# Kernel optimization log

Hardware: AMD Instinct MI355X
Metric: run time of the kernel (lower is better)

Reference implementation:

```python
import jax, jax.numpy as jnp
import numpy as np

N_NODES = 50000
N_EDGES = 800000
IN_DIM = 128
HID = 256
N_CLASSES = 10
N_GRAPHS = 64
BN_EPS = 1e-5


def setup_inputs() -> dict:
    key = jax.random.key(0)
    ks = jax.random.split(key, 12)
    x = jax.random.normal(ks[0], (N_NODES, IN_DIM), dtype=jnp.float32)
    edge_index = jax.random.randint(ks[1], (2, N_EDGES), 0, N_NODES, dtype=jnp.int32)
    batch = jnp.sort(jax.random.randint(ks[2], (N_NODES,), 0, N_GRAPHS, dtype=jnp.int32))
    def glorot(k, fi, fo):
        s = jnp.sqrt(6.0 / (fi + fo))
        return jax.random.uniform(k, (fi, fo), jnp.float32, -s, s)
    return {
        "x": x, "edge_index": edge_index, "batch": batch,
        "W1": glorot(ks[3], IN_DIM, HID), "b1": jnp.zeros((HID,), jnp.float32),
        "W2": glorot(ks[4], HID, HID),    "b2": jnp.zeros((HID,), jnp.float32),
        "W3": glorot(ks[5], HID, HID),    "b3": jnp.zeros((HID,), jnp.float32),
        "g1": jnp.ones((HID,), jnp.float32), "be1": jnp.zeros((HID,), jnp.float32),
        "g2": jnp.ones((HID,), jnp.float32), "be2": jnp.zeros((HID,), jnp.float32),
        "Wf": glorot(ks[6], HID, N_CLASSES), "bf": jnp.zeros((N_CLASSES,), jnp.float32),
    }


def _gcn_conv(h_in, W, b, src, dst, dis):
    # GCNConv: D^{-1/2}(A+I)D^{-1/2} (X W) + b, dis = deg^{-1/2} with self-loops
    h = h_in @ W                                    # [N, C]
    norm = (dis[src] * dis[dst])[:, None]           # [E, 1]
    agg = jax.ops.segment_sum(h[src] * norm, dst, num_segments=N_NODES)
    agg = agg + h * (dis * dis)[:, None]            # self-loop contribution
    return agg + b


def _batch_norm(h, gamma, beta):
    mu = jnp.mean(h, axis=0)
    var = jnp.mean(jnp.square(h - mu), axis=0)      # biased, as torch training BN
    return (h - mu) * jax.lax.rsqrt(var + BN_EPS) * gamma + beta


def reference(x, edge_index, batch, W1, b1, W2, b2, W3, b3, g1, be1, g2, be2, Wf, bf):
    src, dst = edge_index[0], edge_index[1]
    # symmetric degree with self-loops (unit edge weights)
    deg = 1.0 + jax.ops.segment_sum(jnp.ones((N_EDGES,), jnp.float32), dst, num_segments=N_NODES)
    dis = jax.lax.rsqrt(deg)
    h = jax.nn.relu(_gcn_conv(x, W1, b1, src, dst, dis))
    h = jax.nn.relu(_gcn_conv(h, W2, b2, src, dst, dis))
    h = _batch_norm(h, g1, be1)
    h = jax.nn.relu(_gcn_conv(h, W3, b3, src, dst, dis))
    h = _batch_norm(h, g2, be2)
    # global mean pool over graphs
    sums = jax.ops.segment_sum(h, batch, num_segments=N_GRAPHS)
    cnts = jax.ops.segment_sum(jnp.ones((N_NODES,), jnp.float32), batch, num_segments=N_GRAPHS)
    pooled = sums / jnp.maximum(cnts, 1.0)[:, None]  # [G, HID]
    return pooled @ Wf + bf
```

## Files before the change

### kernel.cpp

```cpp
#include <hip/hip_runtime.h>

#define N_NODES 50000
#define N_EDGES 800000
#define IN_DIM 128
#define HID 256
#define N_CLASSES 10
#define N_GRAPHS 64
#define BN_EPS 1e-5f
#define NCHUNK ((N_NODES + 255) / 256)

typedef _Float16 f16x8 __attribute__((ext_vector_type(8)));
typedef _Float16 f16x4 __attribute__((ext_vector_type(4)));
typedef float f32x4 __attribute__((ext_vector_type(4)));

__global__ __launch_bounds__(256) void zero_f4(float4* __restrict__ p, int n4) {
    int i = blockIdx.x * blockDim.x + threadIdx.x;
    int stride = gridDim.x * blockDim.x;
    for (; i < n4; i += stride) p[i] = make_float4(0.f, 0.f, 0.f, 0.f);
}

__global__ __launch_bounds__(256) void count_deg(const int* __restrict__ dst,
                                                 int* __restrict__ deg) {
    int e = blockIdx.x * blockDim.x + threadIdx.x;
    if (e < N_EDGES) atomicAdd(&deg[dst[e]], 1);
}

__global__ __launch_bounds__(256) void deg_to_dis(const int* __restrict__ deg,
                                                  float* __restrict__ dis) {
    int i = blockIdx.x * blockDim.x + threadIdx.x;
    if (i < N_NODES) dis[i] = rsqrtf(1.0f + (float)deg[i]);
}

__global__ __launch_bounds__(256) void scan_chunk(const int* __restrict__ deg,
                                                  int* __restrict__ row_start,
                                                  int* __restrict__ chunk_sums) {
    __shared__ int buf[256];
    int t = threadIdx.x;
    int i = blockIdx.x * 256 + t;
    int v = (i < N_NODES) ? deg[i] : 0;
    buf[t] = v;
    __syncthreads();
#pragma unroll
    for (int off = 1; off < 256; off <<= 1) {
        int tmp = (t >= off) ? buf[t - off] : 0;
        __syncthreads();
        buf[t] += tmp;
        __syncthreads();
    }
    if (i < N_NODES) row_start[i] = buf[t] - v;
    if (t == 255) chunk_sums[blockIdx.x] = buf[255];
}

__global__ __launch_bounds__(256) void scan_tops(int* __restrict__ chunk_sums) {
    __shared__ int buf[256];
    int t = threadIdx.x;
    int v = (t < NCHUNK) ? chunk_sums[t] : 0;
    buf[t] = v;
    __syncthreads();
#pragma unroll
    for (int off = 1; off < 256; off <<= 1) {
        int tmp = (t >= off) ? buf[t - off] : 0;
        __syncthreads();
        buf[t] += tmp;
        __syncthreads();
    }
    if (t < NCHUNK) chunk_sums[t] = buf[t] - v;
}

__global__ __launch_bounds__(256) void scan_add(int* __restrict__ row_start,
                                                const int* __restrict__ chunk_sums) {
    int i = blockIdx.x * blockDim.x + threadIdx.x;
    if (i < N_NODES) row_start[i] += chunk_sums[i >> 8];
}

__global__ __launch_bounds__(256) void fill_adj(const int* __restrict__ src,
                                                const int* __restrict__ dst,
                                                int* __restrict__ row_start,
                                                int* __restrict__ adj) {
    int e = blockIdx.x * blockDim.x + threadIdx.x;
    if (e < N_EDGES) {
        int pos = atomicAdd(&row_start[dst[e]], 1);
        pos = min(pos, N_EDGES - 1);
        adj[pos] = src[e];
    }
}

template<int K>
__global__ __launch_bounds__(256) void gemm_mfma(
    const float* __restrict__ A, const float* __restrict__ W,
    const float* __restrict__ dis, _Float16* __restrict__ out, int M)
{
    __shared__ alignas(16) _Float16 Bs[64][264];
    __shared__ alignas(16) _Float16 As[64][40];

    const int t    = threadIdx.x;
    const int wv   = t >> 6;
    const int lane = t & 63;
    const int row0 = blockIdx.x * 64;
    const int col0 = blockIdx.y * 64;

    {
        const int nc = (t & 7) * 8;
        for (int k = t >> 3; k < K; k += 32) {
            float4 w0 = *(const float4*)(W + (size_t)k * HID + col0 + nc);
            float4 w1 = *(const float4*)(W + (size_t)k * HID + col0 + nc + 4);
            Bs[nc + 0][k] = (_Float16)w0.x;
            Bs[nc + 1][k] = (_Float16)w0.y;
            Bs[nc + 2][k] = (_Float16)w0.z;
            Bs[nc + 3][k] = (_Float16)w0.w;
            Bs[nc + 4][k] = (_Float16)w1.x;
            Bs[nc + 5][k] = (_Float16)w1.y;
            Bs[nc + 6][k] = (_Float16)w1.z;
            Bs[nc + 7][k] = (_Float16)w1.w;
        }
    }
    __syncthreads();

    constexpr int NK = K / 32;
    f16x8 bfr[NK];
#pragma unroll
    for (int s = 0; s < NK; ++s)
        bfr[s] = *(const f16x8*)&Bs[wv * 16 + (lane & 15)][s * 32 + (lane >> 4) * 8];

    f32x4 acc[4] = {};

    const int ar = t >> 2;
    const int ac = (t & 3) * 8;

#pragma unroll
    for (int s = 0; s < NK; ++s) {
        const int k0 = s * 32;
        float4 a0 = make_float4(0.f, 0.f, 0.f, 0.f);
        float4 a1 = make_float4(0.f, 0.f, 0.f, 0.f);
        int gr = row0 + ar;
        if (gr < M) {
            a0 = *(const float4*)(A + (size_t)gr * K + k0 + ac);
            a1 = *(const float4*)(A + (size_t)gr * K + k0 + ac + 4);
        }
        __syncthreads();
        f16x8 av;
        av[0] = (_Float16)a0.x; av[1] = (_Float16)a0.y;
        av[2] = (_Float16)a0.z; av[3] = (_Float16)a0.w;
        av[4] = (_Float16)a1.x; av[5] = (_Float16)a1.y;
        av[6] = (_Float16)a1.z; av[7] = (_Float16)a1.w;
        *(f16x8*)&As[ar][ac] = av;
        __syncthreads();
#pragma unroll
        for (int m = 0; m < 4; ++m) {
            f16x8 af = *(const f16x8*)&As[m * 16 + (lane & 15)][(lane >> 4) * 8];
            acc[m] = __builtin_amdgcn_mfma_f32_16x16x32_f16(af, bfr[s], acc[m], 0, 0, 0);
        }
    }

#pragma unroll
    for (int m = 0; m < 4; ++m) {
#pragma unroll
        for (int i = 0; i < 4; ++i) {
            int r = row0 + m * 16 + (lane >> 4) * 4 + i;
            if (r < M) {
                out[(size_t)r * HID + col0 + wv * 16 + (lane & 15)] =
                    (_Float16)(acc[m][i] * dis[r]);
            }
        }
    }
}

__global__ __launch_bounds__(256) void gather_relu(
    const _Float16* __restrict__ ht, const int* __restrict__ row_end,
    const int* __restrict__ adj, const float* __restrict__ dis,
    const float* __restrict__ b, float* __restrict__ s)
{
    int wid  = (blockIdx.x * 256 + threadIdx.x) >> 6;
    int lane = threadIdx.x & 63;
    if (wid >= N_NODES) return;
    const int n = wid;
    const int c = lane * 4;
    int beg = (n == 0) ? 0 : row_end[n - 1];
    int end = row_end[n];

    f16x4 sv = *(const f16x4*)(ht + (size_t)n * HID + c);
    float4 acc = make_float4((float)sv[0], (float)sv[1], (float)sv[2], (float)sv[3]);

    int j = beg;
    while (j < end) {
        int m = end - j;
        if (m > 64) m = 64;
        int ul = adj[j + (lane < m ? lane : m - 1)];
        ul = min(ul, N_NODES - 1);
        int k = 0;
        for (; k + 1 < m; k += 2) {
            int u0 = __shfl(ul, k);
            int u1 = __shfl(ul, k + 1);
            f16x4 v0 = *(const f16x4*)(ht + (size_t)u0 * HID + c);
            f16x4 v1 = *(const f16x4*)(ht + (size_t)u1 * HID + c);
            acc.x += (float)v0[0] + (float)v1[0];
            acc.y += (float)v0[1] + (float)v1[1];
            acc.z += (float)v0[2] + (float)v1[2];
            acc.w += (float)v0[3] + (float)v1[3];
        }
        if (k < m) {
            int u0 = __shfl(ul, k);
            f16x4 v0 = *(const f16x4*)(ht + (size_t)u0 * HID + c);
            acc.x += (float)v0[0];
            acc.y += (float)v0[1];
            acc.z += (float)v0[2];
            acc.w += (float)v0[3];
        }
        j += m;
    }

    float d = dis[n];
    float4 bv = ((const float4*)b)[lane];
    float4 o;
    o.x = fmaxf(fmaf(d, acc.x, bv.x), 0.f);
    o.y = fmaxf(fmaf(d, acc.y, bv.y), 0.f);
    o.z = fmaxf(fmaf(d, acc.z, bv.z), 0.f);
    o.w = fmaxf(fmaf(d, acc.w, bv.w), 0.f);
    *(float4*)(s + (size_t)n * HID + c) = o;
}

__global__ __launch_bounds__(256) void bn_stats(
    const float* __restrict__ h, float* __restrict__ stats, int rows_per_block)
{
    int c  = threadIdx.x;
    int r0 = blockIdx.x * rows_per_block;
    int r1 = min(r0 + rows_per_block, N_NODES);
    if (r0 >= N_NODES) return;
    float sum = 0.f, sq = 0.f;
    for (int r = r0; r < r1; ++r) {
        float v = h[(size_t)r * HID + c];
        sum += v;
        sq  = fmaf(v, v, sq);
    }
    atomicAdd(&stats[c], sum);
    atomicAdd(&stats[HID + c], sq);
}

__global__ __launch_bounds__(256) void bn_apply(
    float* __restrict__ h, const float* __restrict__ stats,
    const float* __restrict__ g, const float* __restrict__ be)
{
    int idx = blockIdx.x * blockDim.x + threadIdx.x;
    const int total = N_NODES * (HID / 4);
    if (idx >= total) return;
    int c4 = idx & 63;
    const float invN = 1.0f / N_NODES;
    float4 sm = ((const float4*)stats)[c4];
    float4 sq = ((const float4*)(stats + HID))[c4];
    float4 gv = ((const float4*)g)[c4];
    float4 bv = ((const float4*)be)[c4];
    float4 v  = ((float4*)h)[idx];
    float4 o;
    float mu, var, sc;
    mu = sm.x * invN; var = sq.x * invN - mu * mu; sc = rsqrtf(var + BN_EPS) * gv.x;
    o.x = (v.x - mu) * sc + bv.x;
    mu = sm.y * invN; var = sq.y * invN - mu * mu; sc = rsqrtf(var + BN_EPS) * gv.y;
    o.y = (v.y - mu) * sc + bv.y;
    mu = sm.z * invN; var = sq.z * invN - mu * mu; sc = rsqrtf(var + BN_EPS) * gv.z;
    o.z = (v.z - mu) * sc + bv.z;
    mu = sm.w * invN; var = sq.w * invN - mu * mu; sc = rsqrtf(var + BN_EPS) * gv.w;
    o.w = (v.w - mu) * sc + bv.w;
    ((float4*)h)[idx] = o;
}

__global__ __launch_bounds__(256) void pool_accum(
    const float* __restrict__ h, const int* __restrict__ batch,
    float* __restrict__ pool, float* __restrict__ cnt, int rows_per_block)
{
    int c  = threadIdx.x;
    int r0 = blockIdx.x * rows_per_block;
    int r1 = min(r0 + rows_per_block, N_NODES);
    if (r0 >= N_NODES) return;
    float acc = 0.f;
    int curg = batch[r0];
    for (int r = r0; r < r1; ++r) {
        int gidx = batch[r];
        if (gidx != curg) {
            atomicAdd(&pool[(size_t)curg * HID + c], acc);
            acc = 0.f;
            curg = gidx;
        }
        acc += h[(size_t)r * HID + c];
    }
    atomicAdd(&pool[(size_t)curg * HID + c], acc);
    if (c == 0) {
        int cacc = 0;
        int cg = batch[r0];
        for (int r = r0; r < r1; ++r) {
            int gidx = batch[r];
            if (gidx != cg) { atomicAdd(&cnt[cg], (float)cacc); cacc = 0; cg = gidx; }
            cacc++;
        }
        atomicAdd(&cnt[cg], (float)cacc);
    }
}

__global__ __launch_bounds__(256) void final_head(
    const float* __restrict__ pool, const float* __restrict__ cnt,
    const float* __restrict__ Wf, const float* __restrict__ bf,
    float* __restrict__ out)
{
    __shared__ float p[HID];
    int g = blockIdx.x;
    int c = threadIdx.x;
    float inv = 1.0f / fmaxf(cnt[g], 1.0f);
    p[c] = pool[(size_t)g * HID + c] * inv;
    __syncthreads();
    if (c < N_CLASSES) {
        float acc = bf[c];
        for (int k = 0; k < HID; ++k) acc = fmaf(p[k], Wf[k * N_CLASSES + c], acc);
        out[g * N_CLASSES + c] = acc;
    }
}

extern "C" void kernel_launch(void* const* d_in, const int* in_sizes, int n_in,
                              void* d_out, int out_size, void* d_ws, size_t ws_size,
                              hipStream_t stream) {
    const float* x   = (const float*)d_in[0];
    const int* eidx  = (const int*)d_in[1];
    const int* batch = (const int*)d_in[2];
    const float* W1  = (const float*)d_in[3];
    const float* b1  = (const float*)d_in[4];
    const float* W2  = (const float*)d_in[5];
    const float* b2  = (const float*)d_in[6];
    const float* W3  = (const float*)d_in[7];
    const float* b3  = (const float*)d_in[8];
    const float* g1  = (const float*)d_in[9];
    const float* be1 = (const float*)d_in[10];
    const float* g2  = (const float*)d_in[11];
    const float* be2 = (const float*)d_in[12];
    const float* Wf  = (const float*)d_in[13];
    const float* bf  = (const float*)d_in[14];
    float* out = (float*)d_out;

    const int* src = eidx;
    const int* dst = eidx + N_EDGES;

    _Float16* ht     = (_Float16*)d_ws;
    float* s         = (float*)(ht + (size_t)N_NODES * HID);
    float* dis       = s + (size_t)N_NODES * HID;
    float* stats     = dis + N_NODES;
    float* pool      = stats + 2 * HID;
    float* cnt       = pool + (size_t)N_GRAPHS * HID;
    int* deg         = (int*)(cnt + N_GRAPHS);
    int* row_start   = deg + N_NODES;
    int* chunk_sums  = row_start + N_NODES;
    int* adj         = chunk_sums + 256;

    const int feat4   = N_NODES * (HID / 4);
    const int featBlk = (feat4 + 255) / 256;
    const int mTiles  = (N_NODES + 63) / 64;
    dim3 gemmGrid(mTiles, HID / 64);
    const int nodeBlk = (N_NODES + 255) / 256;
    const int edgeBlk = (N_EDGES + 255) / 256;
    const int gatherBlk = (N_NODES * 64 + 255) / 256;
    const int rowsPerBlock = (N_NODES + 255) / 256;

    zero_f4<<<(N_NODES / 4 + 255) / 256, 256, 0, stream>>>((float4*)deg, N_NODES / 4);
    count_deg<<<edgeBlk, 256, 0, stream>>>(dst, deg);
    deg_to_dis<<<nodeBlk, 256, 0, stream>>>(deg, dis);
    scan_chunk<<<NCHUNK, 256, 0, stream>>>(deg, row_start, chunk_sums);
    scan_tops<<<1, 256, 0, stream>>>(chunk_sums);
    scan_add<<<nodeBlk, 256, 0, stream>>>(row_start, chunk_sums);
    fill_adj<<<edgeBlk, 256, 0, stream>>>(src, dst, row_start, adj);

    gemm_mfma<IN_DIM><<<gemmGrid, 256, 0, stream>>>(x, W1, dis, ht, N_NODES);
    gather_relu<<<gatherBlk, 256, 0, stream>>>(ht, row_start, adj, dis, b1, s);

    gemm_mfma<HID><<<gemmGrid, 256, 0, stream>>>(s, W2, dis, ht, N_NODES);
    gather_relu<<<gatherBlk, 256, 0, stream>>>(ht, row_start, adj, dis, b2, s);
    zero_f4<<<1, 256, 0, stream>>>((float4*)stats, 2 * HID / 4);
    bn_stats<<<256, 256, 0, stream>>>(s, stats, rowsPerBlock);
    bn_apply<<<featBlk, 256, 0, stream>>>(s, stats, g1, be1);

    gemm_mfma<HID><<<gemmGrid, 256, 0, stream>>>(s, W3, dis, ht, N_NODES);
    gather_relu<<<gatherBlk, 256, 0, stream>>>(ht, row_start, adj, dis, b3, s);
    zero_f4<<<1, 256, 0, stream>>>((float4*)stats, 2 * HID / 4);
    bn_stats<<<256, 256, 0, stream>>>(s, stats, rowsPerBlock);
    bn_apply<<<featBlk, 256, 0, stream>>>(s, stats, g2, be2);

    zero_f4<<<(N_GRAPHS * HID / 4 + N_GRAPHS / 4 + 255) / 256, 256, 0, stream>>>(
        (float4*)pool, N_GRAPHS * HID / 4 + N_GRAPHS / 4);
    pool_accum<<<256, 256, 0, stream>>>(s, batch, pool, cnt, rowsPerBlock);
    final_head<<<N_GRAPHS, 256, 0, stream>>>(pool, cnt, Wf, bf, out);
}
```

Before: 720.3 us.

## Fold batch-norm apply into next GEMM and pooled head, widen reductions

Measured after the change: 675.2 us. -6.3%, faster.

```diff
diff --git a/kernel.cpp b/kernel.cpp
--- a/kernel.cpp
+++ b/kernel.cpp
@@ -25,15 +25,10 @@
     if (e < N_EDGES) atomicAdd(&deg[dst[e]], 1);
 }
 
-__global__ __launch_bounds__(256) void deg_to_dis(const int* __restrict__ deg,
-                                                  float* __restrict__ dis) {
-    int i = blockIdx.x * blockDim.x + threadIdx.x;
-    if (i < N_NODES) dis[i] = rsqrtf(1.0f + (float)deg[i]);
-}
-
 __global__ __launch_bounds__(256) void scan_chunk(const int* __restrict__ deg,
                                                   int* __restrict__ row_start,
-                                                  int* __restrict__ chunk_sums) {
+                                                  int* __restrict__ chunk_sums,
+                                                  float* __restrict__ dis) {
     __shared__ int buf[256];
     int t = threadIdx.x;
     int i = blockIdx.x * 256 + t;
@@ -47,7 +42,10 @@
         buf[t] += tmp;
         __syncthreads();
     }
-    if (i < N_NODES) row_start[i] = buf[t] - v;
+    if (i < N_NODES) {
+        row_start[i] = buf[t] - v;
+        dis[i] = rsqrtf(1.0f + (float)v);
+    }
     if (t == 255) chunk_sums[blockIdx.x] = buf[255];
 }
 
@@ -85,10 +83,12 @@
     }
 }
 
-template<int K>
+template<int K, bool BN>
 __global__ __launch_bounds__(256) void gemm_mfma(
     const float* __restrict__ A, const float* __restrict__ W,
-    const float* __restrict__ dis, _Float16* __restrict__ out, int M)
+    const float* __restrict__ dis, const float* __restrict__ stats,
+    const float* __restrict__ g, const float* __restrict__ be,
+    _Float16* __restrict__ out, int M)
 {
     __shared__ alignas(16) _Float16 Bs[64][264];
     __shared__ alignas(16) _Float16 As[64][40];
@@ -126,6 +126,7 @@
 
     const int ar = t >> 2;
     const int ac = (t & 3) * 8;
+    const float invN = 1.0f / N_NODES;
 
 #pragma unroll
     for (int s = 0; s < NK; ++s) {
@@ -136,6 +137,34 @@
         if (gr < M) {
             a0 = *(const float4*)(A + (size_t)gr * K + k0 + ac);
             a1 = *(const float4*)(A + (size_t)gr * K + k0 + ac + 4);
+        }
+        if constexpr (BN) {
+            const int kc = k0 + ac;
+            float4 sm0 = *(const float4*)(stats + kc);
+            float4 sm1 = *(const float4*)(stats + kc + 4);
+            float4 sq0 = *(const float4*)(stats + HID + kc);
+            float4 sq1 = *(const float4*)(stats + HID + kc + 4);
+            float4 gv0 = *(const float4*)(g + kc);
+            float4 gv1 = *(const float4*)(g + kc + 4);
+            float4 bv0 = *(const float4*)(be + kc);
+            float4 bv1 = *(const float4*)(be + kc + 4);
+            float mu, var, sc;
+            mu = sm0.x * invN; var = sq0.x * invN - mu * mu;
+            sc = rsqrtf(var + BN_EPS) * gv0.x; a0.x = (a0.x - mu) * sc + bv0.x;
+            mu = sm0.y * invN; var = sq0.y * invN - mu * mu;
+            sc = rsqrtf(var + BN_EPS) * gv0.y; a0.y = (a0.y - mu) * sc + bv0.y;
+            mu = sm0.z * invN; var = sq0.z * invN - mu * mu;
+            sc = rsqrtf(var + BN_EPS) * gv0.z; a0.z = (a0.z - mu) * sc + bv0.z;
+            mu = sm0.w * invN; var = sq0.w * invN - mu * mu;
+            sc = rsqrtf(var + BN_EPS) * gv0.w; a0.w = (a0.w - mu) * sc + bv0.w;
+            mu = sm1.x * invN; var = sq1.x * invN - mu * mu;
+            sc = rsqrtf(var + BN_EPS) * gv1.x; a1.x = (a1.x - mu) * sc + bv1.x;
+            mu = sm1.y * invN; var = sq1.y * invN - mu * mu;
+            sc = rsqrtf(var + BN_EPS) * gv1.y; a1.y = (a1.y - mu) * sc + bv1.y;
+            mu = sm1.z * invN; var = sq1.z * invN - mu * mu;
+            sc = rsqrtf(var + BN_EPS) * gv1.z; a1.z = (a1.z - mu) * sc + bv1.z;
+            mu = sm1.w * invN; var = sq1.w * invN - mu * mu;
+            sc = rsqrtf(var + BN_EPS) * gv1.w; a1.w = (a1.w - mu) * sc + bv1.w;
         }
         __syncthreads();
         f16x8 av;
@@ -236,33 +265,6 @@
     atomicAdd(&stats[HID + c], sq);
 }
 
-__global__ __launch_bounds__(256) void bn_apply(
-    float* __restrict__ h, const float* __restrict__ stats,
-    const float* __restrict__ g, const float* __restrict__ be)
-{
-    int idx = blockIdx.x * blockDim.x + threadIdx.x;
-    const int total = N_NODES * (HID / 4);
-    if (idx >= total) return;
-    int c4 = idx & 63;
-    const float invN = 1.0f / N_NODES;
-    float4 sm = ((const float4*)stats)[c4];
-    float4 sq = ((const float4*)(stats + HID))[c4];
-    float4 gv = ((const float4*)g)[c4];
-    float4 bv = ((const float4*)be)[c4];
-    float4 v  = ((float4*)h)[idx];
-    float4 o;
-    float mu, var, sc;
-    mu = sm.x * invN; var = sq.x * invN - mu * mu; sc = rsqrtf(var + BN_EPS) * gv.x;
-    o.x = (v.x - mu) * sc + bv.x;
-    mu = sm.y * invN; var = sq.y * invN - mu * mu; sc = rsqrtf(var + BN_EPS) * gv.y;
-    o.y = (v.y - mu) * sc + bv.y;
-    mu = sm.z * invN; var = sq.z * invN - mu * mu; sc = rsqrtf(var + BN_EPS) * gv.z;
-    o.z = (v.z - mu) * sc + bv.z;
-    mu = sm.w * invN; var = sq.w * invN - mu * mu; sc = rsqrtf(var + BN_EPS) * gv.w;
-    o.w = (v.w - mu) * sc + bv.w;
-    ((float4*)h)[idx] = o;
-}
-
 __global__ __launch_bounds__(256) void pool_accum(
     const float* __restrict__ h, const int* __restrict__ batch,
     float* __restrict__ pool, float* __restrict__ cnt, int rows_per_block)
@@ -297,19 +299,24 @@
 
 __global__ __launch_bounds__(256) void final_head(
     const float* __restrict__ pool, const float* __restrict__ cnt,
-    const float* __restrict__ Wf, const float* __restrict__ bf,
-    float* __restrict__ out)
+    const float* __restrict__ stats, const float* __restrict__ g2,
+    const float* __restrict__ be2, const float* __restrict__ Wf,
+    const float* __restrict__ bf, float* __restrict__ out)
 {
     __shared__ float p[HID];
-    int g = blockIdx.x;
+    int gb = blockIdx.x;
     int c = threadIdx.x;
-    float inv = 1.0f / fmaxf(cnt[g], 1.0f);
-    p[c] = pool[(size_t)g * HID + c] * inv;
+    const float invN = 1.0f / N_NODES;
+    float inv = 1.0f / fmaxf(cnt[gb], 1.0f);
+    float mu  = stats[c] * invN;
+    float var = stats[HID + c] * invN - mu * mu;
+    float sc  = rsqrtf(var + BN_EPS) * g2[c];
+    p[c] = (pool[(size_t)gb * HID + c] * inv - mu) * sc + be2[c];
     __syncthreads();
     if (c < N_CLASSES) {
         float acc = bf[c];
         for (int k = 0; k < HID; ++k) acc = fmaf(p[k], Wf[k * N_CLASSES + c], acc);
-        out[g * N_CLASSES + c] = acc;
+        out[gb * N_CLASSES + c] = acc;
     }
 }
 
@@ -347,40 +354,39 @@
     int* chunk_sums  = row_start + N_NODES;
     int* adj         = chunk_sums + 256;
 
-    const int feat4   = N_NODES * (HID / 4);
-    const int featBlk = (feat4 + 255) / 256;
     const int mTiles  = (N_NODES + 63) / 64;
     dim3 gemmGrid(mTiles, HID / 64);
     const int nodeBlk = (N_NODES + 255) / 256;
     const int edgeBlk = (N_EDGES + 255) / 256;
     const int gatherBlk = (N_NODES * 64 + 255) / 256;
-    const int rowsPerBlock = (N_NODES + 255) / 256;
+    const int redRows = 25;
+    const int redBlk  = (N_NODES + redRows - 1) / redRows;
 
     zero_f4<<<(N_NODES / 4 + 255) / 256, 256, 0, stream>>>((float4*)deg, N_NODES / 4);
     count_deg<<<edgeBlk, 256, 0, stream>>>(dst, deg);
-    deg_to_dis<<<nodeBlk, 256, 0, stream>>>(deg, dis);
-    scan_chunk<<<NCHUNK, 256, 0, stream>>>(deg, row_start, chunk_sums);
+    scan_chunk<<<NCHUNK, 256, 0, stream>>>(deg, row_start, chunk_sums, dis);
     scan_tops<<<1, 256, 0, stream>>>(chunk_sums);
     scan_add<<<nodeBlk, 256, 0, stream>>>(row_start, chunk_sums);
     fill_adj<<<edgeBlk, 256, 0, stream>>>(src, dst, row_start, adj);
 
-    gemm_mfma<IN_DIM><<<gemmGrid, 256, 0, stream>>>(x, W1, dis, ht, N_NODES);
+    gemm_mfma<IN_DIM, false><<<gemmGrid, 256, 0, stream>>>(
+        x, W1, dis, nullptr, nullptr, nullptr, ht, N_NODES);
     gather_relu<<<gatherBlk, 256, 0, stream>>>(ht, row_start, adj, dis, b1, s);
 
-    gemm_mfma<HID><<<gemmGrid, 256, 0, stream>>>(s, W2, dis, ht, N_NODES);
+    gemm_mfma<HID, false><<<gemmGrid, 256, 0, stream>>>(
+        s, W2, dis, nullptr, nullptr, nullptr, ht, N_NODES);
     gather_relu<<<gatherBlk, 256, 0, stream>>>(ht, row_start, adj, dis, b2, s);
     zero_f4<<<1, 256, 0, stream>>>((float4*)stats, 2 * HID / 4);
-    bn_stats<<<256, 256, 0, stream>>>(s, stats, rowsPerBlock);
-    bn_apply<<<featBlk, 256, 0, stream>>>(s, stats, g1, be1);
-
-    gemm_mfma<HID><<<gemmGrid, 256, 0, stream>>>(s, W3, dis, ht, N_NODES);
+    bn_stats<<<redBlk, 256, 0, stream>>>(s, stats, redRows);
+
+    gemm_mfma<HID, true><<<gemmGrid, 256, 0, stream>>>(
+        s, W3, dis, stats, g1, be1, ht, N_NODES);
     gather_relu<<<gatherBlk, 256, 0, stream>>>(ht, row_start, adj, dis, b3, s);
     zero_f4<<<1, 256, 0, stream>>>((float4*)stats, 2 * HID / 4);
-    bn_stats<<<256, 256, 0, stream>>>(s, stats, rowsPerBlock);
-    bn_apply<<<featBlk, 256, 0, stream>>>(s, stats, g2, be2);
+    bn_stats<<<redBlk, 256, 0, stream>>>(s, stats, redRows);
 
     zero_f4<<<(N_GRAPHS * HID / 4 + N_GRAPHS / 4 + 255) / 256, 256, 0, stream>>>(
         (float4*)pool, N_GRAPHS * HID / 4 + N_GRAPHS / 4);
-    pool_accum<<<256, 256, 0, stream>>>(s, batch, pool, cnt, rowsPerBlock);
-    final_head<<<N_GRAPHS, 256, 0, stream>>>(pool, cnt, Wf, bf, out);
-}
+    pool_accum<<<redBlk, 256, 0, stream>>>(s, batch, pool, cnt, redRows);
+    final_head<<<N_GRAPHS, 256, 0, stream>>>(pool, cnt, stats, g2, be2, Wf, bf, out);
+}
```
